# Optimization experiments

Measured on AMD Instinct MI355X. Metric: run time of the kernel, lower is better.

Reference implementation:

```python
import jax, jax.numpy as jnp
from jax import lax
import numpy as np

N_ASSETS = 256
BATCH = 512
MAX_WEIGHT = 0.05
N_ITERS = 300       # FISTA iterations (fixed, jit-friendly)
BISECT_ITERS = 60   # bisection iterations for the simplex-box projection
POWER_ITERS = 30    # power iterations for Lipschitz constant


def _project_capped_simplex(v, c):
    """Project rows of v onto {w : sum(w)=1, -c <= w <= c}.

    Finds tau s.t. sum(clip(v - tau, -c, c)) = 1 by bisection (non-diff),
    then recomputes tau exactly from the active-set mask so the projection
    is correctly differentiable (piecewise-linear Jacobian).
    """
    vs = lax.stop_gradient(v)
    lo = jnp.min(vs, axis=-1) - c   # sum = +n*c > 1 here
    hi = jnp.max(vs, axis=-1) + c   # sum = -n*c < 1 here

    def bis(carry, _):
        lo, hi = carry
        mid = 0.5 * (lo + hi)
        s = jnp.sum(jnp.clip(vs - mid[:, None], -c, c), axis=-1)
        lo = jnp.where(s > 1.0, mid, lo)
        hi = jnp.where(s > 1.0, hi, mid)
        return (lo, hi), None

    (lo, hi), _ = lax.scan(bis, (lo, hi), None, length=BISECT_ITERS)
    tau0 = 0.5 * (lo + hi)
    z = vs - tau0[:, None]
    interior = (jnp.abs(z) < c).astype(v.dtype)          # unclipped coords
    k_hi = jnp.sum((z >= c).astype(v.dtype), axis=-1)    # clipped at +c
    k_lo = jnp.sum((z <= -c).astype(v.dtype), axis=-1)   # clipped at -c
    denom = jnp.maximum(jnp.sum(interior, axis=-1), 1.0)
    # exact tau given the (stop-gradient) active set -> correct Jacobian in v
    tau = (jnp.sum(interior * v, axis=-1) + c * (k_hi - k_lo) - 1.0) / denom
    return jnp.clip(v - tau[:, None], -c, c)


def _min_var_weights(covmat_sqrt, c):
    """argmin_w ||A w||^2  s.t. sum(w)=1, -c<=w<=c  (batched FISTA)."""
    B, n, _ = covmat_sqrt.shape
    # Q = A^T A (the objective only depends on A through Q)
    Q = jnp.einsum('bij,bik->bjk', covmat_sqrt, covmat_sqrt)

    # power iteration for lambda_max(Q) -> step size 1/L, L = 2*lambda_max
    u = jnp.ones((B, n), covmat_sqrt.dtype) / jnp.sqrt(jnp.asarray(n, covmat_sqrt.dtype))

    def pit(u, _):
        u = jnp.einsum('bij,bj->bi', Q, u)
        u = u / (jnp.linalg.norm(u, axis=-1, keepdims=True) + 1e-12)
        return u, None

    u, _ = lax.scan(pit, u, None, length=POWER_ITERS)
    lmax = jnp.einsum('bi,bij,bj->b', u, Q, u)
    step = lax.stop_gradient(1.0 / (2.0 * lmax + 1e-12))[:, None]

    w0 = _project_capped_simplex(jnp.full((B, n), 1.0 / n, covmat_sqrt.dtype), c)

    @jax.checkpoint
    def fista(carry, _):
        w, y, t = carry
        g = 2.0 * jnp.einsum('bij,bj->bi', Q, y)
        w_new = _project_capped_simplex(y - step * g, c)
        t_new = 0.5 * (1.0 + jnp.sqrt(1.0 + 4.0 * t * t))
        y_new = w_new + ((t - 1.0) / t_new) * (w_new - w)
        return (w_new, y_new, t_new), None

    t0 = jnp.asarray(1.0, covmat_sqrt.dtype)
    (w, _, _), _ = lax.scan(fista, (w0, w0, t0), None, length=N_ITERS)
    return w


def setup_inputs() -> dict:
    key = jax.random.key(0)
    covmat_sqrt = jax.random.normal(
        key, (BATCH, N_ASSETS, N_ASSETS), dtype=jnp.float32
    ) / np.sqrt(N_ASSETS).astype(np.float32)
    return {"covmat_sqrt": covmat_sqrt}


def reference(covmat_sqrt):
    return _min_var_weights(covmat_sqrt, MAX_WEIGHT)
```

## Files before the change

kernel.cpp:

```cpp
#include <hip/hip_runtime.h>
#include <math.h>


#define NA    256
#define CAPW  0.05f

typedef float v2f __attribute__((ext_vector_type(2)));

template<int CTRL, int RM>
__device__ __forceinline__ float dpp0(float x) {
    return __int_as_float(__builtin_amdgcn_update_dpp(
        0, __float_as_int(x), CTRL, RM, 0xf, true));
}
template<int CTRL, int RM>
__device__ __forceinline__ float dppI(float x, float ident) {
    return __int_as_float(__builtin_amdgcn_update_dpp(
        __float_as_int(ident), __float_as_int(x), CTRL, RM, 0xf, false));
}
__device__ __forceinline__ float bcast63(float x) {
    return __int_as_float(__builtin_amdgcn_readlane(__float_as_int(x), 63));
}
__device__ __forceinline__ float wsum(float x) {
    x += dpp0<0x111, 0xf>(x);
    x += dpp0<0x112, 0xf>(x);
    x += dpp0<0x114, 0xf>(x);
    x += dpp0<0x118, 0xf>(x);
    x += dpp0<0x142, 0xa>(x);
    x += dpp0<0x143, 0xc>(x);
    return bcast63(x);
}
__device__ __forceinline__ float wmin(float x) {
    const float I = 1e30f;
    x = fminf(x, dppI<0x111, 0xf>(x, I));
    x = fminf(x, dppI<0x112, 0xf>(x, I));
    x = fminf(x, dppI<0x114, 0xf>(x, I));
    x = fminf(x, dppI<0x118, 0xf>(x, I));
    x = fminf(x, dppI<0x142, 0xa>(x, I));
    x = fminf(x, dppI<0x143, 0xc>(x, I));
    return bcast63(x);
}
__device__ __forceinline__ float wmax(float x) {
    const float I = -1e30f;
    x = fmaxf(x, dppI<0x111, 0xf>(x, I));
    x = fmaxf(x, dppI<0x112, 0xf>(x, I));
    x = fmaxf(x, dppI<0x114, 0xf>(x, I));
    x = fmaxf(x, dppI<0x118, 0xf>(x, I));
    x = fmaxf(x, dppI<0x142, 0xa>(x, I));
    x = fmaxf(x, dppI<0x143, 0xc>(x, I));
    return bcast63(x);
}

#define FOR_CC(M) M(0) M(1) M(2) M(3) M(4) M(5) M(6) M(7)

#define QDECL(cc) \
    v2f q0_##cc##L = {0,0}, q0_##cc##H = {0,0}, \
        q1_##cc##L = {0,0}, q1_##cc##H = {0,0}, \
        q2_##cc##L = {0,0}, q2_##cc##H = {0,0}, \
        q3_##cc##L = {0,0}, q3_##cc##H = {0,0};

#define QBUILD(cc) { \
    float4 cv = *(const float4*)(row + C0 + 4*cc); \
    v2f clo = {cv.x, cv.y}, chi = {cv.z, cv.w}; \
    q0_##cc##L = __builtin_elementwise_fma(r0s, clo, q0_##cc##L); \
    q0_##cc##H = __builtin_elementwise_fma(r0s, chi, q0_##cc##H); \
    q1_##cc##L = __builtin_elementwise_fma(r1s, clo, q1_##cc##L); \
    q1_##cc##H = __builtin_elementwise_fma(r1s, chi, q1_##cc##H); \
    q2_##cc##L = __builtin_elementwise_fma(r2s, clo, q2_##cc##L); \
    q2_##cc##H = __builtin_elementwise_fma(r2s, chi, q2_##cc##H); \
    q3_##cc##L = __builtin_elementwise_fma(r3s, clo, q3_##cc##L); \
    q3_##cc##H = __builtin_elementwise_fma(r3s, chi, q3_##cc##H); }

#define QMV(cc) { \
    float4 y4 = *(const float4*)(yv + 4*cc); \
    v2f ylo = {y4.x, y4.y}, yhi = {y4.z, y4.w}; \
    aL0 = __builtin_elementwise_fma(q0_##cc##L, ylo, aL0); \
    aH0 = __builtin_elementwise_fma(q0_##cc##H, yhi, aH0); \
    aL1 = __builtin_elementwise_fma(q1_##cc##L, ylo, aL1); \
    aH1 = __builtin_elementwise_fma(q1_##cc##H, yhi, aH1); \
    aL2 = __builtin_elementwise_fma(q2_##cc##L, ylo, aL2); \
    aH2 = __builtin_elementwise_fma(q2_##cc##H, yhi, aH2); \
    aL3 = __builtin_elementwise_fma(q3_##cc##L, ylo, aL3); \
    aH3 = __builtin_elementwise_fma(q3_##cc##H, yhi, aH3); }

#define PARTIALS() do { \
    __syncthreads(); \
    v2f aL0={0,0},aH0={0,0},aL1={0,0},aH1={0,0}; \
    v2f aL2={0,0},aH2={0,0},aL3={0,0},aH3={0,0}; \
    const float* yv = y_lds + C0; \
    FOR_CC(QMV) \
    v2f s0 = aL0+aH0, s1 = aL1+aH1, s2 = aL2+aH2, s3 = aL3+aH3; \
    *(float4*)(p_lds + e*256 + R0) = \
        make_float4(s0.x+s0.y, s1.x+s1.y, s2.x+s2.y, s3.x+s3.y); \
    __syncthreads(); \
} while (0)

__global__ void __launch_bounds__(512, 2)
markowitz_fista(const float* __restrict__ A, float* __restrict__ out)
{
    __shared__ float A_lds[32 * 256];
    __shared__ float y_lds[256];
    __shared__ float p_lds[8 * 256];
    __shared__ int   done_flag;

    const int tid  = threadIdx.x;
    const int b    = blockIdx.x;
    const int lane = tid & 63;
    const int e    = tid >> 6;
    const int R0   = lane * 4;
    const int C0   = e * 32;

    const float* __restrict__ Ab = A + (size_t)b * NA * NA;

    FOR_CC(QDECL)

    for (int it = 0; it < 8; ++it) {
        __syncthreads();
        const float4* src = (const float4*)(Ab + it * 32 * 256);
        float4* dst = (float4*)A_lds;
        #pragma unroll
        for (int qd = 0; qd < 4; ++qd) dst[qd * 512 + tid] = src[qd * 512 + tid];
        __syncthreads();
        for (int ii = 0; ii < 32; ++ii) {
            const float* row = A_lds + ii * 256;
            float4 rv = *(const float4*)(row + R0);
            v2f r0s = {rv.x, rv.x}, r1s = {rv.y, rv.y};
            v2f r2s = {rv.z, rv.z}, r3s = {rv.w, rv.w};
            FOR_CC(QBUILD)
        }
    }

    if (tid < 64) {
        *(float4*)(y_lds + R0) = make_float4(0.0625f, 0.0625f, 0.0625f, 0.0625f);
    }
    float u0 = 0.f, u1 = 0.f, u2 = 0.f, u3 = 0.f;
    for (int p = 0; p < 30; ++p) {
        PARTIALS();
        if (tid < 64) {
            float4 g4 = *(const float4*)(p_lds + R0);
            #pragma unroll
            for (int ee = 1; ee < 8; ++ee) {
                float4 pv = *(const float4*)(p_lds + ee * 256 + R0);
                g4.x += pv.x; g4.y += pv.y; g4.z += pv.z; g4.w += pv.w;
            }
            float ss = wsum(g4.x*g4.x + g4.y*g4.y + g4.z*g4.z + g4.w*g4.w);
            float inv = 1.0f / (sqrtf(ss) + 1e-12f);
            u0 = g4.x * inv; u1 = g4.y * inv; u2 = g4.z * inv; u3 = g4.w * inv;
            *(float4*)(y_lds + R0) = make_float4(u0, u1, u2, u3);
        }
    }
    PARTIALS();

    float step2 = 0.f, t = 1.0f, tau_ws = 0.0f, rm = 0.0f;
    float wa = 0.f, wb = 0.f, wc = 0.f, wd = 0.f;
    float ya = 0.f, yb = 0.f, yc = 0.f, yd = 0.f;
    if (tid < 64) {
        float4 g4 = *(const float4*)(p_lds + R0);
        #pragma unroll
        for (int ee = 1; ee < 8; ++ee) {
            float4 pv = *(const float4*)(p_lds + ee * 256 + R0);
            g4.x += pv.x; g4.y += pv.y; g4.z += pv.z; g4.w += pv.w;
        }
        float lm = wsum(u0*g4.x + u1*g4.y + u2*g4.z + u3*g4.w);
        float step = 1.0f / (2.0f * lm + 1e-12f);
        step2 = 2.0f * step;
        wa = wb = wc = wd = 1.0f / 256.0f;
        ya = yb = yc = yd = 1.0f / 256.0f;
        *(float4*)(y_lds + R0) = make_float4(ya, yb, yc, yd);
    }
    if (tid == 0) done_flag = 0;

    for (int itn = 0; itn < 300; ++itn) {
        __syncthreads();
        if (done_flag) break;
        {
            v2f aL0={0,0},aH0={0,0},aL1={0,0},aH1={0,0};
            v2f aL2={0,0},aH2={0,0},aL3={0,0},aH3={0,0};
            const float* yv = y_lds + C0;
            FOR_CC(QMV)
            v2f s0 = aL0+aH0, s1 = aL1+aH1, s2 = aL2+aH2, s3 = aL3+aH3;
            *(float4*)(p_lds + e*256 + R0) =
                make_float4(s0.x+s0.y, s1.x+s1.y, s2.x+s2.y, s3.x+s3.y);
        }
        __syncthreads();

        if (tid < 64) {
            float4 g4 = *(const float4*)(p_lds + R0);
            #pragma unroll
            for (int ee = 1; ee < 8; ++ee) {
                float4 pv = *(const float4*)(p_lds + ee * 256 + R0);
                g4.x += pv.x; g4.y += pv.y; g4.z += pv.z; g4.w += pv.w;
            }
            float v0 = ya - step2 * g4.x;
            float v1 = yb - step2 * g4.y;
            float v2 = yc - step2 * g4.z;
            float v3 = yd - step2 * g4.w;

            float lo = wmin(fminf(fminf(v0, v1), fminf(v2, v3))) - CAPW;
            float hi = wmax(fmaxf(fmaxf(v0, v1), fmaxf(v2, v3))) + CAPW;
            float tau = fminf(fmaxf(tau_ws, lo), hi);

            float s = 0.f, cnt = 1.f, sm1 = 0.f;
            bool have = false;
            for (int ni = 0; ni < 10; ++ni) {
                float z0 = v0 - tau, z1 = v1 - tau, z2 = v2 - tau, z3 = v3 - tau;
                float c0 = fminf(fmaxf(z0, -CAPW), CAPW);
                float c1 = fminf(fmaxf(z1, -CAPW), CAPW);
                float c2 = fminf(fmaxf(z2, -CAPW), CAPW);
                float c3 = fminf(fmaxf(z3, -CAPW), CAPW);
                s   = wsum(c0 + c1 + c2 + c3);
                cnt = wsum((fabsf(z0) < CAPW ? 1.f : 0.f) +
                           (fabsf(z1) < CAPW ? 1.f : 0.f) +
                           (fabsf(z2) < CAPW ? 1.f : 0.f) +
                           (fabsf(z3) < CAPW ? 1.f : 0.f));
                sm1 = s - 1.0f;
                if (fabsf(sm1) <= 1e-5f) { have = true; break; }
                if (sm1 > 0.0f) lo = tau; else hi = tau;
                float tn2 = tau + sm1 / fmaxf(cnt, 1.0f);
                if (!(tn2 > lo && tn2 < hi)) tn2 = 0.5f * (lo + hi);
                tau = tn2;
            }
            if (!have) {
                float z0 = v0 - tau, z1 = v1 - tau, z2 = v2 - tau, z3 = v3 - tau;
                float c0 = fminf(fmaxf(z0, -CAPW), CAPW);
                float c1 = fminf(fmaxf(z1, -CAPW), CAPW);
                float c2 = fminf(fmaxf(z2, -CAPW), CAPW);
                float c3 = fminf(fmaxf(z3, -CAPW), CAPW);
                s   = wsum(c0 + c1 + c2 + c3);
                cnt = wsum((fabsf(z0) < CAPW ? 1.f : 0.f) +
                           (fabsf(z1) < CAPW ? 1.f : 0.f) +
                           (fabsf(z2) < CAPW ? 1.f : 0.f) +
                           (fabsf(z3) < CAPW ? 1.f : 0.f));
                sm1 = s - 1.0f;
            }
            float tauf = tau + sm1 / fmaxf(cnt, 1.0f);
            tau_ws = tauf;
            float w0n = fminf(fmaxf(v0 - tauf, -CAPW), CAPW);
            float w1n = fminf(fmaxf(v1 - tauf, -CAPW), CAPW);
            float w2n = fminf(fmaxf(v2 - tauf, -CAPW), CAPW);
            float w3n = fminf(fmaxf(v3 - tauf, -CAPW), CAPW);

            float tn = 0.5f * (1.0f + sqrtf(1.0f + 4.0f * t * t));
            float beta = (t - 1.0f) / tn;
            float y0n = w0n + beta * (w0n - wa);
            float y1n = w1n + beta * (w1n - wb);
            float y2n = w2n + beta * (w2n - wc);
            float y3n = w3n + beta * (w3n - wd);

            float dm = fmaxf(fmaxf(fabsf(w0n - wa), fabsf(w1n - wb)),
                             fmaxf(fabsf(w2n - wc), fabsf(w3n - wd)));
            rm = fmaxf(rm, dm);
            if ((itn & 7) == 7) {
                float rmax = wmax(rm);
                if (rmax < 1e-10f && tid == 0) done_flag = 1;
                rm = 0.0f;
            }

            wa = w0n; wb = w1n; wc = w2n; wd = w3n;
            ya = y0n; yb = y1n; yc = y2n; yd = y3n;
            t = tn;
            *(float4*)(y_lds + R0) = make_float4(ya, yb, yc, yd);
        }
    }

    if (tid < 64) {
        *(float4*)(out + b * 256 + R0) = make_float4(wa, wb, wc, wd);
    }
}

extern "C" void kernel_launch(void* const* d_in, const int* in_sizes, int n_in,
                              void* d_out, int out_size, void* d_ws, size_t ws_size,
                              hipStream_t stream) {
    (void)in_sizes; (void)n_in; (void)d_ws; (void)ws_size; (void)out_size;
    const float* A = (const float*)d_in[0];
    float* out = (float*)d_out;
    hipLaunchKernelGGL(markowitz_fista, dim3(512), dim3(512), 0, stream, A, out);
}
```

Before: 1.072 ms.

## Split register-resident Q across 16 waves with 1024-thread blocks

Doubles the block to 1024 threads (16 waves), so each wave keeps a 16-column slice of Q in registers instead of 32 columns. This halves per-thread register use and per-wave matvec work in each FISTA and power iteration. The cost is a longer serial reduction of 16 partial vectors by the single projection wave and more LDS for partials. Per-iteration latency is dominated by the serial projection on one wave, so the benefit may be limited.

```diff
diff --git a/kernel.cpp b/kernel.cpp
--- a/kernel.cpp
+++ b/kernel.cpp
@@ -50,7 +50,7 @@
     return bcast63(x);
 }
 
-#define FOR_CC(M) M(0) M(1) M(2) M(3) M(4) M(5) M(6) M(7)
+#define FOR_CC(M) M(0) M(1) M(2) M(3)
 
 #define QDECL(cc) \
     v2f q0_##cc##L = {0,0}, q0_##cc##H = {0,0}, \
@@ -94,12 +94,21 @@
     __syncthreads(); \
 } while (0)
 
-__global__ void __launch_bounds__(512, 2)
+#define REDUCEG(g4) do { \
+    g4 = *(const float4*)(p_lds + R0); \
+    _Pragma("unroll") \
+    for (int ee = 1; ee < 16; ++ee) { \
+        float4 pv = *(const float4*)(p_lds + ee * 256 + R0); \
+        g4.x += pv.x; g4.y += pv.y; g4.z += pv.z; g4.w += pv.w; \
+    } \
+} while (0)
+
+__global__ void __launch_bounds__(1024, 4)
 markowitz_fista(const float* __restrict__ A, float* __restrict__ out)
 {
     __shared__ float A_lds[32 * 256];
     __shared__ float y_lds[256];
-    __shared__ float p_lds[8 * 256];
+    __shared__ float p_lds[16 * 256];
     __shared__ int   done_flag;
 
     const int tid  = threadIdx.x;
@@ -107,7 +116,7 @@
     const int lane = tid & 63;
     const int e    = tid >> 6;
     const int R0   = lane * 4;
-    const int C0   = e * 32;
+    const int C0   = e * 16;
 
     const float* __restrict__ Ab = A + (size_t)b * NA * NA;
 
@@ -118,7 +127,7 @@
         const float4* src = (const float4*)(Ab + it * 32 * 256);
         float4* dst = (float4*)A_lds;
         #pragma unroll
-        for (int qd = 0; qd < 4; ++qd) dst[qd * 512 + tid] = src[qd * 512 + tid];
+        for (int qd = 0; qd < 2; ++qd) dst[qd * 1024 + tid] = src[qd * 1024 + tid];
         __syncthreads();
         for (int ii = 0; ii < 32; ++ii) {
             const float* row = A_lds + ii * 256;
@@ -136,12 +145,7 @@
     for (int p = 0; p < 30; ++p) {
         PARTIALS();
         if (tid < 64) {
-            float4 g4 = *(const float4*)(p_lds + R0);
-            #pragma unroll
-            for (int ee = 1; ee < 8; ++ee) {
-                float4 pv = *(const float4*)(p_lds + ee * 256 + R0);
-                g4.x += pv.x; g4.y += pv.y; g4.z += pv.z; g4.w += pv.w;
-            }
+            float4 g4; REDUCEG(g4);
             float ss = wsum(g4.x*g4.x + g4.y*g4.y + g4.z*g4.z + g4.w*g4.w);
             float inv = 1.0f / (sqrtf(ss) + 1e-12f);
             u0 = g4.x * inv; u1 = g4.y * inv; u2 = g4.z * inv; u3 = g4.w * inv;
@@ -154,12 +158,7 @@
     float wa = 0.f, wb = 0.f, wc = 0.f, wd = 0.f;
     float ya = 0.f, yb = 0.f, yc = 0.f, yd = 0.f;
     if (tid < 64) {
-        float4 g4 = *(const float4*)(p_lds + R0);
-        #pragma unroll
-        for (int ee = 1; ee < 8; ++ee) {
-            float4 pv = *(const float4*)(p_lds + ee * 256 + R0);
-            g4.x += pv.x; g4.y += pv.y; g4.z += pv.z; g4.w += pv.w;
-        }
+        float4 g4; REDUCEG(g4);
         float lm = wsum(u0*g4.x + u1*g4.y + u2*g4.z + u3*g4.w);
         float step = 1.0f / (2.0f * lm + 1e-12f);
         step2 = 2.0f * step;
@@ -184,12 +183,7 @@
         __syncthreads();
 
         if (tid < 64) {
-            float4 g4 = *(const float4*)(p_lds + R0);
-            #pragma unroll
-            for (int ee = 1; ee < 8; ++ee) {
-                float4 pv = *(const float4*)(p_lds + ee * 256 + R0);
-                g4.x += pv.x; g4.y += pv.y; g4.z += pv.z; g4.w += pv.w;
-            }
+            float4 g4; REDUCEG(g4);
             float v0 = ya - step2 * g4.x;
             float v1 = yb - step2 * g4.y;
             float v2 = yc - step2 * g4.z;
@@ -273,5 +267,5 @@
     (void)in_sizes; (void)n_in; (void)d_ws; (void)ws_size; (void)out_size;
     const float* A = (const float*)d_in[0];
     float* out = (float*)d_out;
-    hipLaunchKernelGGL(markowitz_fista, dim3(512), dim3(512), 0, stream, A, out);
-}
+    hipLaunchKernelGGL(markowitz_fista, dim3(512), dim3(1024), 0, stream, A, out);
+}
```

Measured after the change: 1.114 ms. +3.9%, slower.
